# Optimization experiments

Hardware: AMD Instinct MI355X
Metric: run time of the kernel (lower is better)

Reference implementation:

```python
import jax, jax.numpy as jnp
import numpy as np

HIDDEN = 2048
INTER = 5632
N_EXPERTS = 8
TOP_K = 2


def setup_inputs() -> dict:
    key = jax.random.key(0)
    ks = jax.random.split(key, 6)
    x = jax.random.normal(ks[0], (4, 2048, HIDDEN), dtype=jnp.float32)
    router_w = jax.random.normal(ks[1], (N_EXPERTS, HIDDEN), dtype=jnp.float32) * 0.02
    router_b = jnp.zeros((N_EXPERTS,), dtype=jnp.float32)
    Wg = jax.random.normal(ks[2], (N_EXPERTS, INTER, HIDDEN), dtype=jnp.float32) * 0.02
    Wu = jax.random.normal(ks[3], (N_EXPERTS, INTER, HIDDEN), dtype=jnp.float32) * 0.02
    Wd = jax.random.normal(ks[4], (N_EXPERTS, HIDDEN, INTER), dtype=jnp.float32) * 0.02
    return {"x": x, "router_w": router_w, "router_b": router_b, "Wg": Wg, "Wu": Wu, "Wd": Wd}


def reference(x, router_w, router_b, Wg, Wu, Wd):
    batch_shape = x.shape[:-1]
    xf = x.reshape(-1, HIDDEN)  # [T, H]
    T = xf.shape[0]

    # Router: softmax -> top-k -> renormalize (matches torch forward)
    logits = xf @ router_w.T + router_b            # [T, E]
    probs = jax.nn.softmax(logits, axis=-1)
    w, idx = jax.lax.top_k(probs, TOP_K)           # [T, K]
    w = w / jnp.sum(w, axis=-1, keepdims=True)

    # Dense combine weights [T, E]: zero where expert not selected.
    combine = jnp.zeros((T, N_EXPERTS), dtype=xf.dtype)
    combine = combine.at[jnp.arange(T)[:, None], idx].set(w)

    # Weighted sum of SwiGLU expert outputs (loop over fixed small E).
    out = jnp.zeros_like(xf)
    for e in range(N_EXPERTS):
        g = jax.nn.silu(xf @ Wg[e].T)              # [T, I]
        u = xf @ Wu[e].T                           # [T, I]
        h = (g * u) @ Wd[e].T                      # [T, H]
        out = out + combine[:, e:e + 1] * h
    return out.reshape(*batch_shape, HIDDEN)
```

## Files before the change

kernel.cpp:

```cpp
#include <hip/hip_runtime.h>
#include <stdint.h>

#define HID 2048
#define ITR 5632
#define NE 8
#define TT 8192

typedef __attribute__((ext_vector_type(4))) float f4;
typedef __attribute__((ext_vector_type(8))) short s8v;
typedef __attribute__((ext_vector_type(4))) float acc4;
typedef __attribute__((ext_vector_type(4))) unsigned short u4v;
typedef __attribute__((ext_vector_type(8))) unsigned short u8v;
typedef unsigned short ushort_t;

__device__ __forceinline__ unsigned short f2bf(float f) {
    union { float f; uint32_t u; } v; v.f = f;
    uint32_t u = v.u;
    return (unsigned short)((u + 0x7FFFu + ((u >> 16) & 1u)) >> 16);
}

__device__ __forceinline__ void gload16(const unsigned short* g, unsigned short* l) {
    __builtin_amdgcn_global_load_lds(
        (const __attribute__((address_space(1))) unsigned int*)g,
        (__attribute__((address_space(3))) unsigned int*)l, 16, 0, 0);
}

__device__ __forceinline__ int lby(int row, int s) {
    return row * 64 + ((s ^ ((row >> 1) & 3)) * 16);
}

__global__ __launch_bounds__(256) void k_cvt(const float* __restrict__ src,
                                             unsigned short* __restrict__ dst) {
    size_t i = ((size_t)blockIdx.x * 256 + threadIdx.x) * 8;
    f4 a = *(const f4*)(src + i);
    f4 b = *(const f4*)(src + i + 4);
    u8v o;
    o[0]=f2bf(a.x); o[1]=f2bf(a.y); o[2]=f2bf(a.z); o[3]=f2bf(a.w);
    o[4]=f2bf(b.x); o[5]=f2bf(b.y); o[6]=f2bf(b.z); o[7]=f2bf(b.w);
    *(u8v*)(dst + i) = o;
}

#define WBLK 45056
__global__ __launch_bounds__(256) void k_cvtW(const float* __restrict__ a,
                                              const float* __restrict__ b,
                                              const float* __restrict__ c,
                                              unsigned short* __restrict__ oa,
                                              unsigned short* __restrict__ ob,
                                              unsigned short* __restrict__ oc) {
    int bb = blockIdx.x;
    const float* s; unsigned short* d;
    if (bb < WBLK)            { s = a; d = oa; }
    else if (bb < 2 * WBLK)   { s = b; d = ob; bb -= WBLK; }
    else                      { s = c; d = oc; bb -= 2 * WBLK; }
    size_t i = ((size_t)bb * 256 + threadIdx.x) * 8;
    f4 va = *(const f4*)(s + i);
    f4 vb = *(const f4*)(s + i + 4);
    u8v o;
    o[0]=f2bf(va.x); o[1]=f2bf(va.y); o[2]=f2bf(va.z); o[3]=f2bf(va.w);
    o[4]=f2bf(vb.x); o[5]=f2bf(vb.y); o[6]=f2bf(vb.z); o[7]=f2bf(vb.w);
    *(u8v*)(d + i) = o;
}

__global__ __launch_bounds__(256) void k_router(const float* __restrict__ x,
                                                const float* __restrict__ rw,
                                                const float* __restrict__ rb,
                                                int* __restrict__ cnt,
                                                int* __restrict__ tokL,
                                                int* __restrict__ slotL,
                                                float* __restrict__ gateL) {
    int lane = threadIdx.x & 63;
    int wv = threadIdx.x >> 6;
    int t = blockIdx.x * 4 + wv;
    const float* xr = x + (size_t)t * HID;
    float acc[NE];
    #pragma unroll
    for (int e = 0; e < NE; ++e) acc[e] = 0.f;
    #pragma unroll
    for (int i = 0; i < 8; ++i) {
        f4 xv = *(const f4*)(xr + i * 256 + lane * 4);
        #pragma unroll
        for (int e = 0; e < NE; ++e) {
            f4 wv4 = *(const f4*)(rw + e * HID + i * 256 + lane * 4);
            acc[e] += xv.x * wv4.x + xv.y * wv4.y + xv.z * wv4.z + xv.w * wv4.w;
        }
    }
    #pragma unroll
    for (int off = 32; off; off >>= 1)
        #pragma unroll
        for (int e = 0; e < NE; ++e) acc[e] += __shfl_xor(acc[e], off, 64);
    if (lane == 0) {
        float lg[NE];
        #pragma unroll
        for (int e = 0; e < NE; ++e) lg[e] = acc[e] + rb[e];
        int i1 = 0;
        #pragma unroll
        for (int e = 1; e < NE; ++e) if (lg[e] > lg[i1]) i1 = e;
        int i2 = -1;
        #pragma unroll
        for (int e = 0; e < NE; ++e) {
            if (e == i1) continue;
            if (i2 < 0 || lg[e] > lg[i2]) i2 = e;
        }
        float ex = __expf(lg[i2] - lg[i1]);
        float w1 = 1.f / (1.f + ex);
        float w2 = ex / (1.f + ex);
        int p = atomicAdd(&cnt[i1], 1);
        tokL[i1 * TT + p] = t; slotL[i1 * TT + p] = t * 2;     gateL[i1 * TT + p] = w1;
        p = atomicAdd(&cnt[i2], 1);
        tokL[i2 * TT + p] = t; slotL[i2 * TT + p] = t * 2 + 1; gateL[i2 * TT + p] = w2;
    }
}


__global__ __launch_bounds__(512, 2) void k_g1p(const unsigned short* __restrict__ xb,
                                                const unsigned short* __restrict__ WgB,
                                                const unsigned short* __restrict__ WuB,
                                                const int* __restrict__ cnt,
                                                const int* __restrict__ tokL,
                                                const int* __restrict__ slotL,
                                                unsigned short* __restrict__ Hb) {
    int bx = blockIdx.x;
    int e = bx / (32 * 44);
    int r = bx % (32 * 44);
    int mt = r / 44, nt = r % 44;
    int M = cnt[e];
    int m0 = mt * 256;
    if (m0 >= M) return;
    int n0 = nt * 128;

    __shared__ __align__(16) unsigned short lds[65536];
    __shared__ int sTok[256];
    __shared__ int sSlot[256];

    int tid = threadIdx.x;
    if (tid < 256) {
        int m = m0 + tid;
        int mc = m < M ? m : M - 1;
        sTok[tid]  = tokL[e * TT + mc];
        sSlot[tid] = slotL[e * TT + mc];
    }
    __syncthreads();

    int wv = tid >> 6, lane = tid & 63;
    int lrow = lane >> 2;
    int slog = (lane & 3) ^ ((lane >> 3) & 3);

    const unsigned short* aS0 = xb + (size_t)sTok[(2 * wv) * 16 + lrow] * HID + slog * 8;
    const unsigned short* aS1 = xb + (size_t)sTok[(2 * wv + 1) * 16 + lrow] * HID + slog * 8;
    const unsigned short* gS  = WgB + ((size_t)e * ITR + n0 + wv * 16 + lrow) * HID + slog * 8;
    const unsigned short* uS  = WuB + ((size_t)e * ITR + n0 + wv * 16 + lrow) * HID + slog * 8;

    unsigned short* ldsA = lds;
    unsigned short* ldsG = lds + 32768;
    unsigned short* ldsU = lds + 49152;

    auto STAGE = [&](int reg, int kh) {
        int ko = kh * 32;
        gload16(aS0 + ko, ldsA + reg * 8192 + (2 * wv) * 512);
        gload16(aS1 + ko, ldsA + reg * 8192 + (2 * wv + 1) * 512);
        gload16(gS + ko,  ldsG + reg * 4096 + wv * 512);
        gload16(uS + ko,  ldsU + reg * 4096 + wv * 512);
    };

    int wr = wv >> 2, wc = wv & 3;
    int lr = lane & 15, ls = lane >> 4;

    int aOff[8], gOff[2], uOff[2];
    #pragma unroll
    for (int mi = 0; mi < 8; ++mi) aOff[mi] = lby(wr * 128 + mi * 16 + lr, ls);
    #pragma unroll
    for (int ni = 0; ni < 2; ++ni) {
        gOff[ni] = 65536 + lby(wc * 32 + ni * 16 + lr, ls);
        uOff[ni] = 98304 + lby(wc * 32 + ni * 16 + lr, ls);
    }

    acc4 zero4 = {0.f, 0.f, 0.f, 0.f};
    acc4 ag[8][2], au[8][2];
    #pragma unroll
    for (int mi = 0; mi < 8; ++mi)
        #pragma unroll
        for (int ni = 0; ni < 2; ++ni) { ag[mi][ni] = zero4; au[mi][ni] = zero4; }

    STAGE(0, 0); STAGE(1, 1); STAGE(2, 2); STAGE(3, 3);
    asm volatile("s_waitcnt vmcnt(12)" ::: "memory");
    __builtin_amdgcn_s_barrier();

    #pragma unroll 4
    for (int h = 0; h < 64; ++h) {
        int reg = h & 3;
        const char* baseA = (const char*)lds + reg * 16384;
        const char* baseB = (const char*)lds + reg * 8192;
        s8v af[8], gf[2], uf[2];
        #pragma unroll
        for (int mi = 0; mi < 8; ++mi) af[mi] = *(const s8v*)(baseA + aOff[mi]);
        #pragma unroll
        for (int ni = 0; ni < 2; ++ni) {
            gf[ni] = *(const s8v*)(baseB + gOff[ni]);
            uf[ni] = *(const s8v*)(baseB + uOff[ni]);
        }
        asm volatile("s_waitcnt lgkmcnt(0)" ::: "memory");
        __builtin_amdgcn_sched_barrier(0);
        __builtin_amdgcn_s_barrier();
        __builtin_amdgcn_sched_barrier(0);
        int kh = h + 4 < 64 ? h + 4 : 63;
        STAGE(reg, kh);
        __builtin_amdgcn_s_setprio(1);
        #pragma unroll
        for (int mi = 0; mi < 8; ++mi)
            #pragma unroll
            for (int ni = 0; ni < 2; ++ni) {
                ag[mi][ni] = __builtin_amdgcn_mfma_f32_16x16x32_bf16(af[mi], gf[ni], ag[mi][ni], 0, 0, 0);
                au[mi][ni] = __builtin_amdgcn_mfma_f32_16x16x32_bf16(af[mi], uf[ni], au[mi][ni], 0, 0, 0);
            }
        __builtin_amdgcn_s_setprio(0);
        asm volatile("s_waitcnt vmcnt(12)" ::: "memory");
        __builtin_amdgcn_s_barrier();
    }
    asm volatile("s_waitcnt vmcnt(0)" ::: "memory");

    #pragma unroll
    for (int mi = 0; mi < 8; ++mi) {
        #pragma unroll
        for (int j = 0; j < 4; ++j) {
            int m = wr * 128 + mi * 16 + ls * 4 + j;
            if (m0 + m < M) {
                size_t rowOff = (size_t)sSlot[m] * ITR + n0 + wc * 32 + lr;
                #pragma unroll
                for (int ni = 0; ni < 2; ++ni) {
                    float g = ag[mi][ni][j], u = au[mi][ni][j];
                    float h2 = g * (1.f / (1.f + __expf(-g))) * u;
                    Hb[rowOff + ni * 16] = f2bf(h2);
                }
            }
        }
    }
}

__global__ __launch_bounds__(512, 2) void k_g2p(const unsigned short* __restrict__ Hb,
                                                const unsigned short* __restrict__ WdB,
                                                const int* __restrict__ cnt,
                                                const int* __restrict__ tokL,
                                                const int* __restrict__ slotL,
                                                const float* __restrict__ gateL,
                                                float* __restrict__ out) {
    int bx = blockIdx.x;
    int e = bx / (32 * 8);
    int r = bx % (32 * 8);
    int mt = r / 8, nt = r % 8;
    int M = cnt[e];
    int m0 = mt * 256;
    if (m0 >= M) return;
    int n0 = nt * 256;

    __shared__ __align__(16) unsigned short lds[65536];
    __shared__ int sTok[256];
    __shared__ int sSlot[256];
    __shared__ float sGate[256];

    int tid = threadIdx.x;
    if (tid < 256) {
        int m = m0 + tid;
        int mc = m < M ? m : M - 1;
        sTok[tid]  = tokL[e * TT + mc];
        sSlot[tid] = slotL[e * TT + mc];
        sGate[tid] = gateL[e * TT + mc];
    }
    __syncthreads();

    int wv = tid >> 6, lane = tid & 63;
    int lrow = lane >> 2;
    int slog = (lane & 3) ^ ((lane >> 3) & 3);

    const unsigned short* aS0 = Hb + (size_t)sSlot[(2 * wv) * 16 + lrow] * ITR + slog * 8;
    const unsigned short* aS1 = Hb + (size_t)sSlot[(2 * wv + 1) * 16 + lrow] * ITR + slog * 8;
    const unsigned short* bS0 = WdB + ((size_t)e * HID + n0 + (2 * wv) * 16 + lrow) * ITR + slog * 8;
    const unsigned short* bS1 = WdB + ((size_t)e * HID + n0 + (2 * wv + 1) * 16 + lrow) * ITR + slog * 8;

    unsigned short* ldsA = lds;
    unsigned short* ldsB = lds + 32768;

    auto STAGE = [&](int reg, int kh) {
        int ko = kh * 32;
        gload16(aS0 + ko, ldsA + reg * 8192 + (2 * wv) * 512);
        gload16(aS1 + ko, ldsA + reg * 8192 + (2 * wv + 1) * 512);
        gload16(bS0 + ko, ldsB + reg * 8192 + (2 * wv) * 512);
        gload16(bS1 + ko, ldsB + reg * 8192 + (2 * wv + 1) * 512);
    };

    int wr = wv >> 2, wc = wv & 3;
    int lr = lane & 15, ls = lane >> 4;

    int aOff[8], bOff[4];
    #pragma unroll
    for (int mi = 0; mi < 8; ++mi) aOff[mi] = lby(wr * 128 + mi * 16 + lr, ls);
    #pragma unroll
    for (int ni = 0; ni < 4; ++ni) bOff[ni] = 65536 + lby(wc * 64 + ni * 16 + lr, ls);

    acc4 zero4 = {0.f, 0.f, 0.f, 0.f};
    acc4 a4[8][4];
    #pragma unroll
    for (int mi = 0; mi < 8; ++mi)
        #pragma unroll
        for (int ni = 0; ni < 4; ++ni) a4[mi][ni] = zero4;

    STAGE(0, 0); STAGE(1, 1); STAGE(2, 2); STAGE(3, 3);
    asm volatile("s_waitcnt vmcnt(12)" ::: "memory");
    __builtin_amdgcn_s_barrier();

    #pragma unroll 4
    for (int h = 0; h < 176; ++h) {
        int reg = h & 3;
        const char* base = (const char*)lds + reg * 16384;
        s8v af[8], bf[4];
        #pragma unroll
        for (int mi = 0; mi < 8; ++mi) af[mi] = *(const s8v*)(base + aOff[mi]);
        #pragma unroll
        for (int ni = 0; ni < 4; ++ni) bf[ni] = *(const s8v*)(base + bOff[ni]);
        asm volatile("s_waitcnt lgkmcnt(0)" ::: "memory");
        __builtin_amdgcn_sched_barrier(0);
        __builtin_amdgcn_s_barrier();
        __builtin_amdgcn_sched_barrier(0);
        int kh = h + 4 < 176 ? h + 4 : 175;
        STAGE(reg, kh);
        __builtin_amdgcn_s_setprio(1);
        #pragma unroll
        for (int mi = 0; mi < 8; ++mi)
            #pragma unroll
            for (int ni = 0; ni < 4; ++ni)
                a4[mi][ni] = __builtin_amdgcn_mfma_f32_16x16x32_bf16(af[mi], bf[ni], a4[mi][ni], 0, 0, 0);
        __builtin_amdgcn_s_setprio(0);
        asm volatile("s_waitcnt vmcnt(12)" ::: "memory");
        __builtin_amdgcn_s_barrier();
    }
    asm volatile("s_waitcnt vmcnt(0)" ::: "memory");

    #pragma unroll
    for (int mi = 0; mi < 8; ++mi) {
        #pragma unroll
        for (int j = 0; j < 4; ++j) {
            int m = wr * 128 + mi * 16 + ls * 4 + j;
            if (m0 + m < M) {
                int t = sTok[m];
                float w = sGate[m];
                float* orow = out + (size_t)t * HID + n0 + wc * 64 + lr;
                #pragma unroll
                for (int ni = 0; ni < 4; ++ni)
                    atomicAdd(orow + ni * 16, w * a4[mi][ni][j]);
            }
        }
    }
}

#define BM 128
#define BN 128
#define BK 64
#define MT1 64
#define NT1 44
#define NT2 16

__global__ __launch_bounds__(256) void k_gemm1(const unsigned short* __restrict__ xb,
                                               const float* __restrict__ Wg,
                                               const float* __restrict__ Wu,
                                               const int* __restrict__ cnt,
                                               const int* __restrict__ tokL,
                                               const int* __restrict__ slotL,
                                               unsigned short* __restrict__ Hb) {
    int bx = blockIdx.x;
    int e = bx / (MT1 * NT1);
    int r = bx % (MT1 * NT1);
    int mt = r / NT1, nt = r % NT1;
    int M = cnt[e];
    int m0 = mt * BM;
    if (m0 >= M) return;
    int n0 = nt * BN;

    __shared__ __align__(16) unsigned short lA[BM * BK];
    __shared__ __align__(16) unsigned short lBg[BN * BK];
    __shared__ __align__(16) unsigned short lBu[BN * BK];
    __shared__ int sTok[BM];
    __shared__ int sSlot[BM];

    int tid = threadIdx.x;
    if (tid < BM) {
        int m = m0 + tid;
        int mc = m < M ? m : M - 1;
        sTok[tid] = tokL[e * TT + mc];
        sSlot[tid] = slotL[e * TT + mc];
    }
    __syncthreads();

    int ar = tid >> 3, ac = tid & 7;
    const unsigned short* aP[4];
    #pragma unroll
    for (int i = 0; i < 4; ++i)
        aP[i] = xb + (size_t)sTok[ar + 32 * i] * HID + ac * 8;

    int br = tid >> 4, bc = tid & 15;
    const float* gB = Wg + ((size_t)e * ITR + n0) * HID + bc * 4;
    const float* uB = Wu + ((size_t)e * ITR + n0) * HID + bc * 4;

    int wv = tid >> 6, lane = tid & 63;
    int wm = (wv >> 1) * 64, wn = (wv & 1) * 64;
    int lr = lane & 15, lk = (lane >> 4) * 8;

    acc4 zero4 = {0.f, 0.f, 0.f, 0.f};
    acc4 ag[4][4], au[4][4];
    #pragma unroll
    for (int mi = 0; mi < 4; ++mi)
        #pragma unroll
        for (int ni = 0; ni < 4; ++ni) { ag[mi][ni] = zero4; au[mi][ni] = zero4; }

    for (int k0 = 0; k0 < HID; k0 += BK) {
        if (k0) __syncthreads();
        #pragma unroll
        for (int i = 0; i < 4; ++i) {
            int row = ar + 32 * i;
            s8v v = *(const s8v*)(aP[i] + k0);
            int byt = (row * 128 + ac * 16) ^ ((row & 7) << 4);
            *(s8v*)((char*)lA + byt) = v;
        }
        #pragma unroll
        for (int i = 0; i < 8; ++i) {
            int row = br + 16 * i;
            f4 vg = *(const f4*)(gB + (size_t)row * HID + k0);
            f4 vu = *(const f4*)(uB + (size_t)row * HID + k0);
            u4v og = { f2bf(vg.x), f2bf(vg.y), f2bf(vg.z), f2bf(vg.w) };
            u4v ou = { f2bf(vu.x), f2bf(vu.y), f2bf(vu.z), f2bf(vu.w) };
            int byt = (row * 128 + bc * 8) ^ ((row & 7) << 4);
            *(u4v*)((char*)lBg + byt) = og;
            *(u4v*)((char*)lBu + byt) = ou;
        }
        __syncthreads();
        #pragma unroll
        for (int kk = 0; kk < BK; kk += 32) {
            s8v af[4], gf[4], uf[4];
            #pragma unroll
            for (int i = 0; i < 4; ++i) {
                int rowA = wm + i * 16 + lr;
                af[i] = *(const s8v*)((char*)lA + ((rowA * 128 + (kk + lk) * 2) ^ ((rowA & 7) << 4)));
                int rowB = wn + i * 16 + lr;
                int bb = (rowB * 128 + (kk + lk) * 2) ^ ((rowB & 7) << 4);
                gf[i] = *(const s8v*)((char*)lBg + bb);
                uf[i] = *(const s8v*)((char*)lBu + bb);
            }
            #pragma unroll
            for (int mi = 0; mi < 4; ++mi)
                #pragma unroll
                for (int ni = 0; ni < 4; ++ni) {
                    ag[mi][ni] = __builtin_amdgcn_mfma_f32_16x16x32_bf16(af[mi], gf[ni], ag[mi][ni], 0, 0, 0);
                    au[mi][ni] = __builtin_amdgcn_mfma_f32_16x16x32_bf16(af[mi], uf[ni], au[mi][ni], 0, 0, 0);
                }
        }
    }
    #pragma unroll
    for (int mi = 0; mi < 4; ++mi) {
        #pragma unroll
        for (int j = 0; j < 4; ++j) {
            int m = wm + mi * 16 + (lane >> 4) * 4 + j;
            if (m0 + m < M) {
                size_t rowOff = (size_t)sSlot[m] * ITR + n0 + wn + lr;
                #pragma unroll
                for (int ni = 0; ni < 4; ++ni) {
                    float g = ag[mi][ni][j], u = au[mi][ni][j];
                    float h = g * (1.f / (1.f + __expf(-g))) * u;
                    Hb[rowOff + ni * 16] = f2bf(h);
                }
            }
        }
    }
}

__global__ __launch_bounds__(256) void k_gemm2(const unsigned short* __restrict__ Hb,
                                               const float* __restrict__ Wd,
                                               const int* __restrict__ cnt,
                                               const int* __restrict__ tokL,
                                               const int* __restrict__ slotL,
                                               const float* __restrict__ gateL,
                                               float* __restrict__ out) {
    int bx = blockIdx.x;
    int e = bx / (MT1 * NT2);
    int r = bx % (MT1 * NT2);
    int mt = r / NT2, nt = r % NT2;
    int M = cnt[e];
    int m0 = mt * BM;
    if (m0 >= M) return;
    int n0 = nt * BN;

    __shared__ __align__(16) unsigned short lA[BM * BK];
    __shared__ __align__(16) unsigned short lB[BN * BK];
    __shared__ int sTok[BM];
    __shared__ int sSlot[BM];
    __shared__ float sGate[BM];

    int tid = threadIdx.x;
    if (tid < BM) {
        int m = m0 + tid;
        int mc = m < M ? m : M - 1;
        sTok[tid] = tokL[e * TT + mc];
        sSlot[tid] = slotL[e * TT + mc];
        sGate[tid] = gateL[e * TT + mc];
    }
    __syncthreads();

    int ar = tid >> 3, ac = tid & 7;
    const unsigned short* aP[4];
    #pragma unroll
    for (int i = 0; i < 4; ++i)
        aP[i] = Hb + (size_t)sSlot[ar + 32 * i] * ITR + ac * 8;

    int br = tid >> 4, bc = tid & 15;
    const float* dB = Wd + ((size_t)e * HID + n0) * ITR + bc * 4;

    int wv = tid >> 6, lane = tid & 63;
    int wm = (wv >> 1) * 64, wn = (wv & 1) * 64;
    int lr = lane & 15, lk = (lane >> 4) * 8;

    acc4 zero4 = {0.f, 0.f, 0.f, 0.f};
    acc4 a4[4][4];
    #pragma unroll
    for (int mi = 0; mi < 4; ++mi)
        #pragma unroll
        for (int ni = 0; ni < 4; ++ni) a4[mi][ni] = zero4;

    for (int k0 = 0; k0 < ITR; k0 += BK) {
        if (k0) __syncthreads();
        #pragma unroll
        for (int i = 0; i < 4; ++i) {
            int row = ar + 32 * i;
            s8v v = *(const s8v*)(aP[i] + k0);
            int byt = (row * 128 + ac * 16) ^ ((row & 7) << 4);
            *(s8v*)((char*)lA + byt) = v;
        }
        #pragma unroll
        for (int i = 0; i < 8; ++i) {
            int row = br + 16 * i;
            f4 vd = *(const f4*)(dB + (size_t)row * ITR + k0);
            u4v od = { f2bf(vd.x), f2bf(vd.y), f2bf(vd.z), f2bf(vd.w) };
            int byt = (row * 128 + bc * 8) ^ ((row & 7) << 4);
            *(u4v*)((char*)lB + byt) = od;
        }
        __syncthreads();
        #pragma unroll
        for (int kk = 0; kk < BK; kk += 32) {
            s8v af[4], bf[4];
            #pragma unroll
            for (int i = 0; i < 4; ++i) {
                int rowA = wm + i * 16 + lr;
                af[i] = *(const s8v*)((char*)lA + ((rowA * 128 + (kk + lk) * 2) ^ ((rowA & 7) << 4)));
                int rowB = wn + i * 16 + lr;
                bf[i] = *(const s8v*)((char*)lB + ((rowB * 128 + (kk + lk) * 2) ^ ((rowB & 7) << 4)));
            }
            #pragma unroll
            for (int mi = 0; mi < 4; ++mi)
                #pragma unroll
                for (int ni = 0; ni < 4; ++ni)
                    a4[mi][ni] = __builtin_amdgcn_mfma_f32_16x16x32_bf16(af[mi], bf[ni], a4[mi][ni], 0, 0, 0);
        }
    }
    #pragma unroll
    for (int mi = 0; mi < 4; ++mi) {
        #pragma unroll
        for (int j = 0; j < 4; ++j) {
            int m = wm + mi * 16 + (lane >> 4) * 4 + j;
            if (m0 + m < M) {
                int t = sTok[m];
                float w = sGate[m];
                float* orow = out + (size_t)t * HID + n0 + wn + lr;
                #pragma unroll
                for (int ni = 0; ni < 4; ++ni)
                    atomicAdd(orow + ni * 16, w * a4[mi][ni][j]);
            }
        }
    }
}

extern "C" void kernel_launch(void* const* d_in, const int* in_sizes, int n_in,
                              void* d_out, int out_size, void* d_ws, size_t ws_size,
                              hipStream_t stream) {
    const float* x  = (const float*)d_in[0];
    const float* rw = (const float*)d_in[1];
    const float* rb = (const float*)d_in[2];
    const float* Wg = (const float*)d_in[3];
    const float* Wu = (const float*)d_in[4];
    const float* Wd = (const float*)d_in[5];
    float* out = (float*)d_out;
    char* ws = (char*)d_ws;

    const size_t OFF_XB   = 0;
    const size_t OFF_HB   = 33554432ull;
    const size_t OFF_TOK  = 218103808ull;
    const size_t OFF_SLOT = 218365952ull;
    const size_t OFF_GATE = 218628096ull;
    const size_t OFF_CNT  = 218890240ull;
    const size_t OFF_WG   = 218891264ull;
    const size_t OFF_WU   = 403440640ull;
    const size_t OFF_WD   = 587990016ull;
    const size_t NEED     = 772539392ull;

    unsigned short* xb   = (unsigned short*)(ws + OFF_XB);
    unsigned short* Hb   = (unsigned short*)(ws + OFF_HB);
    int*   tokL  = (int*)(ws + OFF_TOK);
    int*   slotL = (int*)(ws + OFF_SLOT);
    float* gateL = (float*)(ws + OFF_GATE);
    int*   cnt   = (int*)(ws + OFF_CNT);

    hipMemsetAsync(cnt, 0, NE * sizeof(int), stream);
    hipMemsetAsync(out, 0, (size_t)out_size * sizeof(float), stream);
    k_cvt<<<8192, 256, 0, stream>>>(x, xb);
    k_router<<<2048, 256, 0, stream>>>(x, rw, rb, cnt, tokL, slotL, gateL);

    if (ws_size >= NEED) {
        unsigned short* WgB = (unsigned short*)(ws + OFF_WG);
        unsigned short* WuB = (unsigned short*)(ws + OFF_WU);
        unsigned short* WdB = (unsigned short*)(ws + OFF_WD);
        k_cvtW<<<3 * WBLK, 256, 0, stream>>>(Wg, Wu, Wd, WgB, WuB, WdB);
        k_g1p<<<NE * 32 * 44, 512, 0, stream>>>(xb, WgB, WuB, cnt, tokL, slotL, Hb);
        k_g2p<<<NE * 32 * 8, 512, 0, stream>>>(Hb, WdB, cnt, tokL, slotL, gateL, out);
    } else {
        k_gemm1<<<NE * MT1 * NT1, 256, 0, stream>>>(xb, Wg, Wu, cnt, tokL, slotL, Hb);
        k_gemm2<<<NE * MT1 * NT2, 256, 0, stream>>>(Hb, Wd, cnt, tokL, slotL, gateL, out);
    }
}
```

Before: 1.938 ms.

## Restructure expert GEMMs into 8-phase ping-pong pipeline with 64-wide K tiles

Both expert GEMM kernels are rewritten to use K tiles of 64 (instead of 32) with a two-buffer LDS scheme split into A/B halves, and an 8-phase schedule per iteration. Each phase interleaves LDS fragment reads, global-to-LDS prefetch of the next tile's halves, and a block of MFMAs, with a new XOR swizzle for the 128-byte rows. The aim is finer-grained overlap of memory loads with matrix math and fewer barriers per unit of work. It adds many barriers and hand-tuned waitcnt values, which risks stalls or subtle ordering bugs.

```diff
diff --git a/kernel.cpp b/kernel.cpp
--- a/kernel.cpp
+++ b/kernel.cpp
@@ -11,7 +11,6 @@
 typedef __attribute__((ext_vector_type(4))) float acc4;
 typedef __attribute__((ext_vector_type(4))) unsigned short u4v;
 typedef __attribute__((ext_vector_type(8))) unsigned short u8v;
-typedef unsigned short ushort_t;
 
 __device__ __forceinline__ unsigned short f2bf(float f) {
     union { float f; uint32_t u; } v; v.f = f;
@@ -25,9 +24,7 @@
         (__attribute__((address_space(3))) unsigned int*)l, 16, 0, 0);
 }
 
-__device__ __forceinline__ int lby(int row, int s) {
-    return row * 64 + ((s ^ ((row >> 1) & 3)) * 16);
-}
+#define MFMA16(a, b, c) __builtin_amdgcn_mfma_f32_16x16x32_bf16(a, b, c, 0, 0, 0)
 
 __global__ __launch_bounds__(256) void k_cvt(const float* __restrict__ src,
                                              unsigned short* __restrict__ dst) {
@@ -112,13 +109,49 @@
 }
 
 
-__global__ __launch_bounds__(512, 2) void k_g1p(const unsigned short* __restrict__ xb,
+#define RD_A(D, MH) { _Pragma("unroll") for (int f2 = 0; f2 < 4; ++f2) { \
+    const char* _b = ldsc + (D)*65536 + aRB + ((MH)*4+f2)*2048; \
+    af[f2*2]   = *(const s8v*)(_b + sw0); \
+    af[f2*2+1] = *(const s8v*)(_b + sw1); } }
+
+#define RD_B(D, BH) { _Pragma("unroll") for (int b2 = 0; b2 < 2; ++b2) { \
+    const char* _b = ldsc + (D)*65536 + bRB + (BH)*16384 + b2*2048; \
+    bf[b2*2]   = *(const s8v*)(_b + sw0); \
+    bf[b2*2+1] = *(const s8v*)(_b + sw1); } }
+
+#define PH_MFMA(MH, BH) \
+    __builtin_amdgcn_s_setprio(1); \
+    { _Pragma("unroll") for (int f2 = 0; f2 < 4; ++f2) \
+      _Pragma("unroll") for (int b2 = 0; b2 < 2; ++b2) { \
+        acc[(MH)*4+f2][(BH)*2+b2] = MFMA16(af[f2*2],   bf[b2*2],   acc[(MH)*4+f2][(BH)*2+b2]); \
+        acc[(MH)*4+f2][(BH)*2+b2] = MFMA16(af[f2*2+1], bf[b2*2+1], acc[(MH)*4+f2][(BH)*2+b2]); } } \
+    __builtin_amdgcn_s_setprio(0);
+
+#define STG_A(D, H, T) { int ko = ((T) < NTK ? (T) : (NTK-1)) * 64; \
+    gload16(pA##H##0 + ko, lds + (D)*32768 + (H)*8192 + tid8); \
+    gload16(pA##H##1 + ko, lds + (D)*32768 + (H)*8192 + 4096 + tid8); }
+
+#define STG_B(D, H, T) { int ko = ((T) < NTK ? (T) : (NTK-1)) * 64; \
+    gload16(pB##H##0 + ko, lds + (D)*32768 + 16384 + (H)*8192 + tid8); \
+    gload16(pB##H##1 + ko, lds + (D)*32768 + 16384 + (H)*8192 + 4096 + tid8); }
+
+#define BAR_LGKM \
+    __builtin_amdgcn_s_barrier(); \
+    asm volatile("s_waitcnt lgkmcnt(0)" ::: "memory");
+
+#define ENDP \
+    __builtin_amdgcn_s_barrier(); \
+    __builtin_amdgcn_sched_barrier(0);
+
+__global__ __launch_bounds__(512, 2) void k_g1r(const unsigned short* __restrict__ xb,
                                                 const unsigned short* __restrict__ WgB,
                                                 const unsigned short* __restrict__ WuB,
                                                 const int* __restrict__ cnt,
                                                 const int* __restrict__ tokL,
                                                 const int* __restrict__ slotL,
                                                 unsigned short* __restrict__ Hb) {
+    constexpr int NTK = 32;
+    constexpr int NI  = 16;
     int bx = blockIdx.x;
     int e = bx / (32 * 44);
     int r = bx % (32 * 44);
@@ -142,107 +175,100 @@
     __syncthreads();
 
     int wv = tid >> 6, lane = tid & 63;
-    int lrow = lane >> 2;
-    int slog = (lane & 3) ^ ((lane >> 3) & 3);
-
-    const unsigned short* aS0 = xb + (size_t)sTok[(2 * wv) * 16 + lrow] * HID + slog * 8;
-    const unsigned short* aS1 = xb + (size_t)sTok[(2 * wv + 1) * 16 + lrow] * HID + slog * 8;
-    const unsigned short* gS  = WgB + ((size_t)e * ITR + n0 + wv * 16 + lrow) * HID + slog * 8;
-    const unsigned short* uS  = WuB + ((size_t)e * ITR + n0 + wv * 16 + lrow) * HID + slog * 8;
-
-    unsigned short* ldsA = lds;
-    unsigned short* ldsG = lds + 32768;
-    unsigned short* ldsU = lds + 49152;
-
-    auto STAGE = [&](int reg, int kh) {
-        int ko = kh * 32;
-        gload16(aS0 + ko, ldsA + reg * 8192 + (2 * wv) * 512);
-        gload16(aS1 + ko, ldsA + reg * 8192 + (2 * wv + 1) * 512);
-        gload16(gS + ko,  ldsG + reg * 4096 + wv * 512);
-        gload16(uS + ko,  ldsU + reg * 4096 + wv * 512);
-    };
+    int tid8 = tid * 8;
+    int srow = wv * 8 + (lane >> 3);
+    int swc = ((lane & 7) ^ ((lane >> 3) & 7)) * 8;
+
+    const unsigned short* pA00 = xb + (size_t)sTok[      srow] * HID + swc;
+    const unsigned short* pA01 = xb + (size_t)sTok[ 64 + srow] * HID + swc;
+    const unsigned short* pA10 = xb + (size_t)sTok[128 + srow] * HID + swc;
+    const unsigned short* pA11 = xb + (size_t)sTok[192 + srow] * HID + swc;
+    const unsigned short* pB00 = WgB + ((size_t)e * ITR + n0 +      srow) * HID + swc;
+    const unsigned short* pB01 = WgB + ((size_t)e * ITR + n0 + 64 + srow) * HID + swc;
+    const unsigned short* pB10 = WuB + ((size_t)e * ITR + n0 +      srow) * HID + swc;
+    const unsigned short* pB11 = WuB + ((size_t)e * ITR + n0 + 64 + srow) * HID + swc;
 
     int wr = wv >> 2, wc = wv & 3;
     int lr = lane & 15, ls = lane >> 4;
-
-    int aOff[8], gOff[2], uOff[2];
-    #pragma unroll
-    for (int mi = 0; mi < 8; ++mi) aOff[mi] = lby(wr * 128 + mi * 16 + lr, ls);
-    #pragma unroll
-    for (int ni = 0; ni < 2; ++ni) {
-        gOff[ni] = 65536 + lby(wc * 32 + ni * 16 + lr, ls);
-        uOff[ni] = 98304 + lby(wc * 32 + ni * 16 + lr, ls);
-    }
-
+    int sw0 = (ls ^ (lr & 7)) * 16;
+    int sw1 = sw0 ^ 64;
+    const char* ldsc = (const char*)lds;
+    int aRB = wr * 16384 + lr * 128;
+    int bRB = 32768 + wc * 4096 + lr * 128;
+
+    s8v af[8], bf[4];
+    acc4 acc[8][4];
     acc4 zero4 = {0.f, 0.f, 0.f, 0.f};
-    acc4 ag[8][2], au[8][2];
-    #pragma unroll
-    for (int mi = 0; mi < 8; ++mi)
-        #pragma unroll
-        for (int ni = 0; ni < 2; ++ni) { ag[mi][ni] = zero4; au[mi][ni] = zero4; }
-
-    STAGE(0, 0); STAGE(1, 1); STAGE(2, 2); STAGE(3, 3);
-    asm volatile("s_waitcnt vmcnt(12)" ::: "memory");
+    #pragma unroll
+    for (int f = 0; f < 8; ++f)
+        #pragma unroll
+        for (int b = 0; b < 4; ++b) acc[f][b] = zero4;
+
+    STG_B(0, 0, 0); STG_B(0, 1, 0); STG_A(0, 0, 0); STG_A(0, 1, 0);
+    STG_B(1, 1, 1); STG_A(1, 0, 1); STG_A(1, 1, 1);
+    asm volatile("s_waitcnt vmcnt(6)" ::: "memory");
     __builtin_amdgcn_s_barrier();
-
-    #pragma unroll 4
-    for (int h = 0; h < 64; ++h) {
-        int reg = h & 3;
-        const char* baseA = (const char*)lds + reg * 16384;
-        const char* baseB = (const char*)lds + reg * 8192;
-        s8v af[8], gf[2], uf[2];
-        #pragma unroll
-        for (int mi = 0; mi < 8; ++mi) af[mi] = *(const s8v*)(baseA + aOff[mi]);
-        #pragma unroll
-        for (int ni = 0; ni < 2; ++ni) {
-            gf[ni] = *(const s8v*)(baseB + gOff[ni]);
-            uf[ni] = *(const s8v*)(baseB + uOff[ni]);
-        }
-        asm volatile("s_waitcnt lgkmcnt(0)" ::: "memory");
-        __builtin_amdgcn_sched_barrier(0);
-        __builtin_amdgcn_s_barrier();
-        __builtin_amdgcn_sched_barrier(0);
-        int kh = h + 4 < 64 ? h + 4 : 63;
-        STAGE(reg, kh);
-        __builtin_amdgcn_s_setprio(1);
-        #pragma unroll
-        for (int mi = 0; mi < 8; ++mi)
-            #pragma unroll
-            for (int ni = 0; ni < 2; ++ni) {
-                ag[mi][ni] = __builtin_amdgcn_mfma_f32_16x16x32_bf16(af[mi], gf[ni], ag[mi][ni], 0, 0, 0);
-                au[mi][ni] = __builtin_amdgcn_mfma_f32_16x16x32_bf16(af[mi], uf[ni], au[mi][ni], 0, 0, 0);
-            }
-        __builtin_amdgcn_s_setprio(0);
-        asm volatile("s_waitcnt vmcnt(12)" ::: "memory");
-        __builtin_amdgcn_s_barrier();
+    __builtin_amdgcn_sched_barrier(0);
+
+    #pragma unroll 1
+    for (int it = 0; it < NI; ++it) {
+        int t1 = 2 * it + 1, t2 = 2 * it + 2, t3 = 2 * it + 3;
+        RD_A(0, 0); RD_B(0, 0);
+        STG_B(1, 0, t1);
+        BAR_LGKM; PH_MFMA(0, 0); ENDP;
+        RD_B(0, 1);
+        BAR_LGKM; PH_MFMA(0, 1); ENDP;
+        RD_A(0, 1);
+        STG_B(0, 1, t2);
+        BAR_LGKM; PH_MFMA(1, 1); ENDP;
+        RD_B(0, 0);
+        STG_A(0, 0, t2);
+        BAR_LGKM; PH_MFMA(1, 0);
+        asm volatile("s_waitcnt vmcnt(4)" ::: "memory");
+        ENDP;
+        RD_A(1, 0); RD_B(1, 0);
+        STG_A(0, 1, t2); STG_B(0, 0, t2);
+        BAR_LGKM; PH_MFMA(0, 0); ENDP;
+        RD_B(1, 1);
+        BAR_LGKM; PH_MFMA(0, 1); ENDP;
+        RD_A(1, 1);
+        STG_B(1, 1, t3);
+        BAR_LGKM; PH_MFMA(1, 1); ENDP;
+        RD_B(1, 0);
+        STG_A(1, 0, t3); STG_A(1, 1, t3);
+        BAR_LGKM; PH_MFMA(1, 0);
+        asm volatile("s_waitcnt vmcnt(6)" ::: "memory");
+        ENDP;
     }
     asm volatile("s_waitcnt vmcnt(0)" ::: "memory");
 
     #pragma unroll
-    for (int mi = 0; mi < 8; ++mi) {
+    for (int f = 0; f < 8; ++f) {
         #pragma unroll
         for (int j = 0; j < 4; ++j) {
-            int m = wr * 128 + mi * 16 + ls * 4 + j;
+            int m = wr * 128 + f * 16 + ls * 4 + j;
             if (m0 + m < M) {
                 size_t rowOff = (size_t)sSlot[m] * ITR + n0 + wc * 32 + lr;
                 #pragma unroll
-                for (int ni = 0; ni < 2; ++ni) {
-                    float g = ag[mi][ni][j], u = au[mi][ni][j];
-                    float h2 = g * (1.f / (1.f + __expf(-g))) * u;
-                    Hb[rowOff + ni * 16] = f2bf(h2);
+                for (int b = 0; b < 2; ++b) {
+                    float g = acc[f][b][j], u = acc[f][b + 2][j];
+                    float h = g * (1.f / (1.f + __expf(-g))) * u;
+                    Hb[rowOff + b * 16] = f2bf(h);
                 }
             }
         }
     }
 }
 
-__global__ __launch_bounds__(512, 2) void k_g2p(const unsigned short* __restrict__ Hb,
+__global__ __launch_bounds__(512, 2) void k_g2r(const unsigned short* __restrict__ Hb,
                                                 const unsigned short* __restrict__ WdB,
                                                 const int* __restrict__ cnt,
                                                 const int* __restrict__ tokL,
                                                 const int* __restrict__ slotL,
                                                 const float* __restrict__ gateL,
                                                 float* __restrict__ out) {
+    constexpr int NTK = 88;
+    constexpr int NI  = 44;
     int bx = blockIdx.x;
     int e = bx / (32 * 8);
     int r = bx % (32 * 8);
@@ -268,84 +294,87 @@
     __syncthreads();
 
     int wv = tid >> 6, lane = tid & 63;
-    int lrow = lane >> 2;
-    int slog = (lane & 3) ^ ((lane >> 3) & 3);
-
-    const unsigned short* aS0 = Hb + (size_t)sSlot[(2 * wv) * 16 + lrow] * ITR + slog * 8;
-    const unsigned short* aS1 = Hb + (size_t)sSlot[(2 * wv + 1) * 16 + lrow] * ITR + slog * 8;
-    const unsigned short* bS0 = WdB + ((size_t)e * HID + n0 + (2 * wv) * 16 + lrow) * ITR + slog * 8;
-    const unsigned short* bS1 = WdB + ((size_t)e * HID + n0 + (2 * wv + 1) * 16 + lrow) * ITR + slog * 8;
-
-    unsigned short* ldsA = lds;
-    unsigned short* ldsB = lds + 32768;
-
-    auto STAGE = [&](int reg, int kh) {
-        int ko = kh * 32;
-        gload16(aS0 + ko, ldsA + reg * 8192 + (2 * wv) * 512);
-        gload16(aS1 + ko, ldsA + reg * 8192 + (2 * wv + 1) * 512);
-        gload16(bS0 + ko, ldsB + reg * 8192 + (2 * wv) * 512);
-        gload16(bS1 + ko, ldsB + reg * 8192 + (2 * wv + 1) * 512);
-    };
+    int tid8 = tid * 8;
+    int srow = wv * 8 + (lane >> 3);
+    int swc = ((lane & 7) ^ ((lane >> 3) & 7)) * 8;
+
+    const unsigned short* pA00 = Hb + (size_t)sSlot[      srow] * ITR + swc;
+    const unsigned short* pA01 = Hb + (size_t)sSlot[ 64 + srow] * ITR + swc;
+    const unsigned short* pA10 = Hb + (size_t)sSlot[128 + srow] * ITR + swc;
+    const unsigned short* pA11 = Hb + (size_t)sSlot[192 + srow] * ITR + swc;
+    const unsigned short* pB00 = WdB + ((size_t)e * HID + n0 +       srow) * ITR + swc;
+    const unsigned short* pB01 = WdB + ((size_t)e * HID + n0 +  64 + srow) * ITR + swc;
+    const unsigned short* pB10 = WdB + ((size_t)e * HID + n0 + 128 + srow) * ITR + swc;
+    const unsigned short* pB11 = WdB + ((size_t)e * HID + n0 + 192 + srow) * ITR + swc;
 
     int wr = wv >> 2, wc = wv & 3;
     int lr = lane & 15, ls = lane >> 4;
-
-    int aOff[8], bOff[4];
-    #pragma unroll
-    for (int mi = 0; mi < 8; ++mi) aOff[mi] = lby(wr * 128 + mi * 16 + lr, ls);
-    #pragma unroll
-    for (int ni = 0; ni < 4; ++ni) bOff[ni] = 65536 + lby(wc * 64 + ni * 16 + lr, ls);
-
+    int sw0 = (ls ^ (lr & 7)) * 16;
+    int sw1 = sw0 ^ 64;
+    const char* ldsc = (const char*)lds;
+    int aRB = wr * 16384 + lr * 128;
+    int bRB = 32768 + wc * 4096 + lr * 128;
+
+    s8v af[8], bf[4];
+    acc4 acc[8][4];
     acc4 zero4 = {0.f, 0.f, 0.f, 0.f};
-    acc4 a4[8][4];
-    #pragma unroll
-    for (int mi = 0; mi < 8; ++mi)
-        #pragma unroll
-        for (int ni = 0; ni < 4; ++ni) a4[mi][ni] = zero4;
-
-    STAGE(0, 0); STAGE(1, 1); STAGE(2, 2); STAGE(3, 3);
-    asm volatile("s_waitcnt vmcnt(12)" ::: "memory");
+    #pragma unroll
+    for (int f = 0; f < 8; ++f)
+        #pragma unroll
+        for (int b = 0; b < 4; ++b) acc[f][b] = zero4;
+
+    STG_B(0, 0, 0); STG_B(0, 1, 0); STG_A(0, 0, 0); STG_A(0, 1, 0);
+    STG_B(1, 1, 1); STG_A(1, 0, 1); STG_A(1, 1, 1);
+    asm volatile("s_waitcnt vmcnt(6)" ::: "memory");
     __builtin_amdgcn_s_barrier();
-
-    #pragma unroll 4
-    for (int h = 0; h < 176; ++h) {
-        int reg = h & 3;
-        const char* base = (const char*)lds + reg * 16384;
-        s8v af[8], bf[4];
-        #pragma unroll
-        for (int mi = 0; mi < 8; ++mi) af[mi] = *(const s8v*)(base + aOff[mi]);
-        #pragma unroll
-        for (int ni = 0; ni < 4; ++ni) bf[ni] = *(const s8v*)(base + bOff[ni]);
-        asm volatile("s_waitcnt lgkmcnt(0)" ::: "memory");
-        __builtin_amdgcn_sched_barrier(0);
-        __builtin_amdgcn_s_barrier();
-        __builtin_amdgcn_sched_barrier(0);
-        int kh = h + 4 < 176 ? h + 4 : 175;
-        STAGE(reg, kh);
-        __builtin_amdgcn_s_setprio(1);
-        #pragma unroll
-        for (int mi = 0; mi < 8; ++mi)
-            #pragma unroll
-            for (int ni = 0; ni < 4; ++ni)
-                a4[mi][ni] = __builtin_amdgcn_mfma_f32_16x16x32_bf16(af[mi], bf[ni], a4[mi][ni], 0, 0, 0);
-        __builtin_amdgcn_s_setprio(0);
-        asm volatile("s_waitcnt vmcnt(12)" ::: "memory");
-        __builtin_amdgcn_s_barrier();
+    __builtin_amdgcn_sched_barrier(0);
+
+    #pragma unroll 1
+    for (int it = 0; it < NI; ++it) {
+        int t1 = 2 * it + 1, t2 = 2 * it + 2, t3 = 2 * it + 3;
+        RD_A(0, 0); RD_B(0, 0);
+        STG_B(1, 0, t1);
+        BAR_LGKM; PH_MFMA(0, 0); ENDP;
+        RD_B(0, 1);
+        BAR_LGKM; PH_MFMA(0, 1); ENDP;
+        RD_A(0, 1);
+        STG_B(0, 1, t2);
+        BAR_LGKM; PH_MFMA(1, 1); ENDP;
+        RD_B(0, 0);
+        STG_A(0, 0, t2);
+        BAR_LGKM; PH_MFMA(1, 0);
+        asm volatile("s_waitcnt vmcnt(4)" ::: "memory");
+        ENDP;
+        RD_A(1, 0); RD_B(1, 0);
+        STG_A(0, 1, t2); STG_B(0, 0, t2);
+        BAR_LGKM; PH_MFMA(0, 0); ENDP;
+        RD_B(1, 1);
+        BAR_LGKM; PH_MFMA(0, 1); ENDP;
+        RD_A(1, 1);
+        STG_B(1, 1, t3);
+        BAR_LGKM; PH_MFMA(1, 1); ENDP;
+        RD_B(1, 0);
+        STG_A(1, 0, t3); STG_A(1, 1, t3);
+        BAR_LGKM; PH_MFMA(1, 0);
+        asm volatile("s_waitcnt vmcnt(6)" ::: "memory");
+        ENDP;
     }
     asm volatile("s_waitcnt vmcnt(0)" ::: "memory");
 
     #pragma unroll
-    for (int mi = 0; mi < 8; ++mi) {
+    for (int f = 0; f < 8; ++f) {
         #pragma unroll
         for (int j = 0; j < 4; ++j) {
-            int m = wr * 128 + mi * 16 + ls * 4 + j;
+            int m = wr * 128 + f * 16 + ls * 4 + j;
             if (m0 + m < M) {
                 int t = sTok[m];
                 float w = sGate[m];
-                float* orow = out + (size_t)t * HID + n0 + wc * 64 + lr;
-                #pragma unroll
-                for (int ni = 0; ni < 4; ++ni)
-                    atomicAdd(orow + ni * 16, w * a4[mi][ni][j]);
+                float* o0 = out + (size_t)t * HID + n0 + wc * 32 + lr;
+                atomicAdd(o0,      w * acc[f][0][j]);
+                atomicAdd(o0 + 16, w * acc[f][1][j]);
+                float* o1 = out + (size_t)t * HID + n0 + 128 + wc * 32 + lr;
+                atomicAdd(o1,      w * acc[f][2][j]);
+                atomicAdd(o1 + 16, w * acc[f][3][j]);
             }
         }
     }
@@ -433,11 +462,11 @@
         __syncthreads();
         #pragma unroll
         for (int kk = 0; kk < BK; kk += 32) {
-            s8v af[4], gf[4], uf[4];
+            s8v af2[4], gf[4], uf[4];
             #pragma unroll
             for (int i = 0; i < 4; ++i) {
                 int rowA = wm + i * 16 + lr;
-                af[i] = *(const s8v*)((char*)lA + ((rowA * 128 + (kk + lk) * 2) ^ ((rowA & 7) << 4)));
+                af2[i] = *(const s8v*)((char*)lA + ((rowA * 128 + (kk + lk) * 2) ^ ((rowA & 7) << 4)));
                 int rowB = wn + i * 16 + lr;
                 int bb = (rowB * 128 + (kk + lk) * 2) ^ ((rowB & 7) << 4);
                 gf[i] = *(const s8v*)((char*)lBg + bb);
@@ -447,8 +476,8 @@
             for (int mi = 0; mi < 4; ++mi)
                 #pragma unroll
                 for (int ni = 0; ni < 4; ++ni) {
-                    ag[mi][ni] = __builtin_amdgcn_mfma_f32_16x16x32_bf16(af[mi], gf[ni], ag[mi][ni], 0, 0, 0);
-                    au[mi][ni] = __builtin_amdgcn_mfma_f32_16x16x32_bf16(af[mi], uf[ni], au[mi][ni], 0, 0, 0);
+                    ag[mi][ni] = MFMA16(af2[mi], gf[ni], ag[mi][ni]);
+                    au[mi][ni] = MFMA16(af2[mi], uf[ni], au[mi][ni]);
                 }
         }
     }
@@ -542,19 +571,19 @@
         __syncthreads();
         #pragma unroll
         for (int kk = 0; kk < BK; kk += 32) {
-            s8v af[4], bf[4];
+            s8v af2[4], bf2[4];
             #pragma unroll
             for (int i = 0; i < 4; ++i) {
                 int rowA = wm + i * 16 + lr;
-                af[i] = *(const s8v*)((char*)lA + ((rowA * 128 + (kk + lk) * 2) ^ ((rowA & 7) << 4)));
+                af2[i] = *(const s8v*)((char*)lA + ((rowA * 128 + (kk + lk) * 2) ^ ((rowA & 7) << 4)));
                 int rowB = wn + i * 16 + lr;
-                bf[i] = *(const s8v*)((char*)lB + ((rowB * 128 + (kk + lk) * 2) ^ ((rowB & 7) << 4)));
+                bf2[i] = *(const s8v*)((char*)lB + ((rowB * 128 + (kk + lk) * 2) ^ ((rowB & 7) << 4)));
             }
             #pragma unroll
             for (int mi = 0; mi < 4; ++mi)
                 #pragma unroll
                 for (int ni = 0; ni < 4; ++ni)
-                    a4[mi][ni] = __builtin_amdgcn_mfma_f32_16x16x32_bf16(af[mi], bf[ni], a4[mi][ni], 0, 0, 0);
+                    a4[mi][ni] = MFMA16(af2[mi], bf2[ni], a4[mi][ni]);
         }
     }
     #pragma unroll
@@ -614,8 +643,8 @@
         unsigned short* WuB = (unsigned short*)(ws + OFF_WU);
         unsigned short* WdB = (unsigned short*)(ws + OFF_WD);
         k_cvtW<<<3 * WBLK, 256, 0, stream>>>(Wg, Wu, Wd, WgB, WuB, WdB);
-        k_g1p<<<NE * 32 * 44, 512, 0, stream>>>(xb, WgB, WuB, cnt, tokL, slotL, Hb);
-        k_g2p<<<NE * 32 * 8, 512, 0, stream>>>(Hb, WdB, cnt, tokL, slotL, gateL, out);
+        k_g1r<<<NE * 32 * 44, 512, 0, stream>>>(xb, WgB, WuB, cnt, tokL, slotL, Hb);
+        k_g2r<<<NE * 32 * 8, 512, 0, stream>>>(Hb, WdB, cnt, tokL, slotL, gateL, out);
     } else {
         k_gemm1<<<NE * MT1 * NT1, 256, 0, stream>>>(xb, Wg, Wu, cnt, tokL, slotL, Hb);
         k_gemm2<<<NE * MT1 * NT2, 256, 0, stream>>>(Hb, Wd, cnt, tokL, slotL, gateL, out);
```

New measurement: 2.030 ms. 4.8% more time.
